# Kernel tuning notes

Measured on AMD Instinct MI355X. Metric: run time of the kernel, lower is better.

The kernel has to match this reference:

```python
import jax, jax.numpy as jnp
import numpy as np


def setup_inputs() -> dict:
    key = jax.random.key(0)
    k1, k2 = jax.random.split(key)
    decoder_output = jax.random.normal(k1, (8, 2048, 128), dtype=jnp.float32)
    encoder_output = jax.random.normal(k2, (8, 4096, 128), dtype=jnp.float32)
    return {"decoder_output": decoder_output, "encoder_output": encoder_output}


def reference(decoder_output, encoder_output):
    # Unscaled Luong (general dot) attention.
    # scores: [B, Tq, Tk] = dec [B,Tq,D] . enc [B,Tk,D]^T
    scores = jnp.einsum('bqd,bkd->bqk', decoder_output, encoder_output)
    attention = jax.nn.softmax(scores, axis=-1)
    # context: [B, Tq, D] = attn [B,Tq,Tk] . enc [B,Tk,D]
    context = jnp.einsum('bqk,bkd->bqd', attention, encoder_output)
    return (context, attention)
```

## Files before the change

### kernel.cpp

```cpp
#include <hip/hip_runtime.h>

using f16   = _Float16;
using f16x4 = __attribute__((ext_vector_type(4))) _Float16;
using f16x8 = __attribute__((ext_vector_type(8))) _Float16;
using f32x4 = __attribute__((ext_vector_type(4))) float;

#define NBATCH 8
#define TQ 2048
#define TK 4096
#define DD 128
#define QBLK 32
#define KBLK 128
#define NT (TK / KBLK)
#define CTX_ELEMS ((size_t)NBATCH * TQ * DD)
#define PWLD 56
#define CTLD 132
#define KTB 36864

__device__ __forceinline__ int koff(int t, int d) {
    const int blk = ((t >> 2) & 3) ^ ((d >> 4) & 3);
    return (t >> 4) * 2304 + (d >> 4) * 288 + blk * 72 + (t & 3) * 16 + (d & 15);
}

__device__ __forceinline__ f16x4 ds_read_tr16(unsigned addr) {
    f16x4 d;
    asm volatile("ds_read_b64_tr_b16 %0, %1" : "=v"(d) : "v"(addr));
    return d;
}

__device__ __forceinline__ void pipe_barrier() {
    asm volatile("s_waitcnt lgkmcnt(0)" ::: "memory");
    __builtin_amdgcn_s_barrier();
    __builtin_amdgcn_sched_barrier(0);
}

__global__ __launch_bounds__(256)
void cvt_kernel(const float* __restrict__ in, f16* __restrict__ out) {
    const size_t i = ((size_t)blockIdx.x * 256 + threadIdx.x) * 8;
    const float4 a = *(const float4*)(in + i);
    const float4 b = *(const float4*)(in + i + 4);
    f16x8 h;
    h[0] = (f16)a.x; h[1] = (f16)a.y; h[2] = (f16)a.z; h[3] = (f16)a.w;
    h[4] = (f16)b.x; h[5] = (f16)b.y; h[6] = (f16)b.z; h[7] = (f16)b.w;
    *(f16x8*)(out + i) = h;
}

template<bool F16SRC>
__global__ __launch_bounds__(512, 4)
void luong_attn_kernel(const float* __restrict__ dec,
                       const void* __restrict__ encv,
                       float* __restrict__ out) {
    __shared__ __align__(16) char LDSbuf[2 * KTB + 512];
    f16*   Kt0   = (f16*)LDSbuf;
    f16*   Kt1   = (f16*)(LDSbuf + KTB);
    f16*   PwAll = (f16*)(LDSbuf + KTB);
    float* Zbuf  = (float*)(LDSbuf + 2 * KTB);

    const int tid  = threadIdx.x;
    const int wid  = tid >> 6;
    const int lane = tid & 63;
    const int lo   = lane & 15;
    const int g    = lane >> 4;
    const int qg   = wid & 1;
    const int th   = wid >> 1;

    const int b     = blockIdx.x & 7;
    const int qbase = (blockIdx.x >> 3) * QBLK;

    const float* encB32 = F16SRC ? nullptr : ((const float*)encv) + (size_t)b * TK * DD;
    const f16*   encB16 = F16SRC ? ((const f16*)encv) + (size_t)b * TK * DD : nullptr;
    float* attn = out + CTX_ELEMS + ((size_t)b * TQ + qbase) * TK;

    f16x8  s16[4];
    float4 s32[8];
    auto loadR = [&](int tile) {
        if constexpr (F16SRC) {
            const f16* src = encB16 + (size_t)tile * KBLK * DD;
            #pragma unroll
            for (int i = 0; i < 4; ++i) {
                const int c = tid + (i << 9);
                s16[i] = *(const f16x8*)(src + (c >> 4) * DD + ((c & 15) << 3));
            }
        } else {
            const float* src = encB32 + (size_t)tile * KBLK * DD;
            #pragma unroll
            for (int i = 0; i < 8; ++i) {
                const int c = tid + (i << 9);
                s32[i] = *(const float4*)(src + (c >> 5) * DD + ((c & 31) << 2));
            }
        }
    };
    auto writeR = [&](f16* Kt) {
        if constexpr (F16SRC) {
            #pragma unroll
            for (int i = 0; i < 4; ++i) {
                const int c = tid + (i << 9);
                *(f16x8*)&Kt[koff(c >> 4, (c & 15) << 3)] = s16[i];
            }
        } else {
            #pragma unroll
            for (int i = 0; i < 8; ++i) {
                const int c = tid + (i << 9);
                f16x4 h;
                h[0] = (f16)s32[i].x; h[1] = (f16)s32[i].y;
                h[2] = (f16)s32[i].z; h[3] = (f16)s32[i].w;
                *(f16x4*)&Kt[koff(c >> 5, (c & 31) << 2)] = h;
            }
        }
    };

    const float* qp = dec + ((size_t)b * TQ + qbase + qg * 16 + lo) * DD;
    f16x8 qf[4];
    #pragma unroll
    for (int kk = 0; kk < 4; ++kk) {
        const float4 x = *(const float4*)(qp + kk * 32 + g * 8);
        const float4 y = *(const float4*)(qp + kk * 32 + g * 8 + 4);
        f16x8 h;
        h[0] = (f16)x.x; h[1] = (f16)x.y; h[2] = (f16)x.z; h[3] = (f16)x.w;
        h[4] = (f16)y.x; h[5] = (f16)y.y; h[6] = (f16)y.z; h[7] = (f16)y.w;
        qf[kk] = h;
    }

    float Zp[4] = {0.f, 0.f, 0.f, 0.f};
    loadR(0);
    writeR(Kt0);
    pipe_barrier();
    #pragma unroll 1
    for (int tile = 0; tile < NT; ++tile) {
        f16* Ktc = (tile & 1) ? Kt1 : Kt0;
        f16* Ktn = (tile & 1) ? Kt0 : Kt1;
        if (tile + 1 < NT) loadR(tile + 1);

        f32x4 S[2];
        #pragma unroll
        for (int f = 0; f < 2; ++f) { f32x4 z = {0.f, 0.f, 0.f, 0.f}; S[f] = z; }
        __builtin_amdgcn_s_setprio(1);
        #pragma unroll
        for (int f = 0; f < 2; ++f) {
            const int t = th * 32 + f * 16 + lo;
            #pragma unroll
            for (int kk = 0; kk < 4; ++kk) {
                const f16x8 bf = *(const f16x8*)&Ktc[koff(t, kk * 32 + g * 8)];
                S[f] = __builtin_amdgcn_mfma_f32_16x16x32_f16(qf[kk], bf, S[f], 0, 0, 0);
            }
        }
        __builtin_amdgcn_s_setprio(0);

        if (tile + 1 < NT) writeR(Ktn);
        #pragma unroll
        for (int r = 0; r < 4; ++r)
            Zp[r] += __expf(S[0][r]) + __expf(S[1][r]);
        pipe_barrier();
    }

    #pragma unroll
    for (int r = 0; r < 4; ++r) {
        Zp[r] += __shfl_xor(Zp[r], 1);
        Zp[r] += __shfl_xor(Zp[r], 2);
        Zp[r] += __shfl_xor(Zp[r], 4);
        Zp[r] += __shfl_xor(Zp[r], 8);
    }
    if (lo == 0) {
        #pragma unroll
        for (int r = 0; r < 4; ++r) Zbuf[wid * 16 + 4 * g + r] = Zp[r];
    }
    __syncthreads();
    float iz[4];
    #pragma unroll
    for (int r = 0; r < 4; ++r) {
        float z = 0.f;
        #pragma unroll
        for (int t4 = 0; t4 < 4; ++t4) z += Zbuf[(t4 * 2 + qg) * 16 + 4 * g + r];
        iz[r] = 1.0f / z;
    }
    __syncthreads();

    f32x4 ctx[8];
    #pragma unroll
    for (int n = 0; n < 8; ++n) { f32x4 z = {0.f, 0.f, 0.f, 0.f}; ctx[n] = z; }

    f16* Pw = PwAll + wid * 16 * PWLD;
    const unsigned KtBase = (unsigned)(size_t)&Kt0[0];
    const int t0 = th * 32 + g * 8;

    #pragma unroll 1
    for (int tile = 0; tile < NT; ++tile) {
        loadR(tile);
        writeR(Kt0);
        pipe_barrier();

        f32x4 S[2];
        #pragma unroll
        for (int f = 0; f < 2; ++f) { f32x4 z = {0.f, 0.f, 0.f, 0.f}; S[f] = z; }
        __builtin_amdgcn_s_setprio(1);
        #pragma unroll
        for (int f = 0; f < 2; ++f) {
            const int t = th * 32 + f * 16 + lo;
            #pragma unroll
            for (int kk = 0; kk < 4; ++kk) {
                const f16x8 bf = *(const f16x8*)&Kt0[koff(t, kk * 32 + g * 8)];
                S[f] = __builtin_amdgcn_mfma_f32_16x16x32_f16(qf[kk], bf, S[f], 0, 0, 0);
            }
        }
        __builtin_amdgcn_s_setprio(0);

        #pragma unroll
        for (int f = 0; f < 2; ++f) {
            const int tloc = f * 16 + lo;
            #pragma unroll
            for (int r = 0; r < 4; ++r)
                Pw[(4 * g + r) * PWLD + tloc] = (f16)(__expf(S[f][r]) * iz[r]);
        }
        asm volatile("" ::: "memory");

        {
            const int qq  = lane >> 2;
            const int grp = lane & 3;
            const f16x8 pr = *(const f16x8*)&Pw[qq * PWLD + grp * 8];
            f32x4 a0, a1;
            a0[0] = (float)pr[0]; a0[1] = (float)pr[1]; a0[2] = (float)pr[2]; a0[3] = (float)pr[3];
            a1[0] = (float)pr[4]; a1[1] = (float)pr[5]; a1[2] = (float)pr[6]; a1[3] = (float)pr[7];
            float* dst = attn + (size_t)(qg * 16 + qq) * TK + tile * KBLK + th * 32 + grp * 8;
            __builtin_nontemporal_store(a0, (f32x4*)dst);
            __builtin_nontemporal_store(a1, (f32x4*)(dst + 4));
        }

        const f16x8 pa = *(const f16x8*)&Pw[lo * PWLD + g * 8];
        __builtin_amdgcn_s_setprio(1);
        #pragma unroll
        for (int nh = 0; nh < 2; ++nh) {
            f16x4 tr0[4], tr1[4];
            #pragma unroll
            for (int n4 = 0; n4 < 4; ++n4) {
                const int n = nh * 4 + n4;
                const int blk0 = ((t0 >> 2) & 3) ^ (n & 3);
                const int blk1 = (((t0 + 4) >> 2) & 3) ^ (n & 3);
                const unsigned a0 =
                    KtBase + (unsigned)(((t0 >> 4) * 2304 + n * 288 + blk0 * 72) * 2) + lo * 8;
                const unsigned a1 =
                    KtBase + (unsigned)(((t0 >> 4) * 2304 + n * 288 + blk1 * 72) * 2) + lo * 8;
                tr0[n4] = ds_read_tr16(a0);
                tr1[n4] = ds_read_tr16(a1);
            }
            asm volatile("s_waitcnt lgkmcnt(0)" ::: "memory");
            __builtin_amdgcn_sched_barrier(0);
            #pragma unroll
            for (int n4 = 0; n4 < 4; ++n4) {
                f16x8 vb;
                vb[0] = tr0[n4][0]; vb[1] = tr0[n4][1]; vb[2] = tr0[n4][2]; vb[3] = tr0[n4][3];
                vb[4] = tr1[n4][0]; vb[5] = tr1[n4][1]; vb[6] = tr1[n4][2]; vb[7] = tr1[n4][3];
                ctx[nh * 4 + n4] =
                    __builtin_amdgcn_mfma_f32_16x16x32_f16(pa, vb, ctx[nh * 4 + n4], 0, 0, 0);
            }
        }
        __builtin_amdgcn_s_setprio(0);
        pipe_barrier();
    }

    float* CT = (float*)LDSbuf;
    const int q32 = qg * 16 + 4 * g;
    if (th >= 2) {
        #pragma unroll
        for (int n = 0; n < 8; ++n)
            #pragma unroll
            for (int r = 0; r < 4; ++r)
                CT[((th - 2) * 32 + q32 + r) * CTLD + n * 16 + lo] = ctx[n][r];
    }
    __syncthreads();
    if (th < 2) {
        #pragma unroll
        for (int n = 0; n < 8; ++n)
            #pragma unroll
            for (int r = 0; r < 4; ++r)
                ctx[n][r] += CT[(th * 32 + q32 + r) * CTLD + n * 16 + lo];
    }
    __syncthreads();
    if (th == 1) {
        #pragma unroll
        for (int n = 0; n < 8; ++n)
            #pragma unroll
            for (int r = 0; r < 4; ++r)
                CT[(q32 + r) * CTLD + n * 16 + lo] = ctx[n][r];
    }
    __syncthreads();
    if (th == 0) {
        #pragma unroll
        for (int n = 0; n < 8; ++n)
            #pragma unroll
            for (int r = 0; r < 4; ++r)
                out[((size_t)b * TQ + qbase + q32 + r) * DD + n * 16 + lo] =
                    ctx[n][r] + CT[(q32 + r) * CTLD + n * 16 + lo];
    }
}

extern "C" void kernel_launch(void* const* d_in, const int* in_sizes, int n_in,
                              void* d_out, int out_size, void* d_ws, size_t ws_size,
                              hipStream_t stream) {
    (void)in_sizes; (void)n_in; (void)out_size;
    const float* dec = (const float*)d_in[0];
    const float* enc = (const float*)d_in[1];
    float* out = (float*)d_out;
    dim3 grid(NBATCH * (TQ / QBLK));
    dim3 block(512);

    const size_t encN = (size_t)NBATCH * TK * DD;
    if (ws_size >= encN * sizeof(f16)) {
        f16* encH = (f16*)d_ws;
        hipLaunchKernelGGL(cvt_kernel, dim3((unsigned)(encN / (256 * 8))), dim3(256),
                           0, stream, enc, encH);
        hipLaunchKernelGGL((luong_attn_kernel<true>), grid, block, 0, stream,
                           dec, (const void*)encH, out);
    } else {
        hipLaunchKernelGGL((luong_attn_kernel<false>), grid, block, 0, stream,
                           dec, (const void*)enc, out);
    }
}
```

Measured before the change: 122.7 us.

## Reuse K fragments across both query halves and prefetch next tile in pass two

In the normalizer pass, each wave now covers 16 keys for both 16-row query halves. Each K fragment read from LDS therefore feeds two MFMAs instead of being read once per query half. In the second pass, the global load of the next K tile is issued after the score computation rather than at the top of the loop, and the first tile's load is started before the Z reduction; one barrier after the reduction is dropped. This should cut LDS traffic in pass one and hide global-load latency in pass two, at the cost of extra registers for the duplicated query fragments and a larger Z buffer.

New measurement: 152.0 us. 1.24x slower.

```diff
diff --git a/kernel.cpp b/kernel.cpp
--- a/kernel.cpp
+++ b/kernel.cpp
@@ -50,7 +50,7 @@
 void luong_attn_kernel(const float* __restrict__ dec,
                        const void* __restrict__ encv,
                        float* __restrict__ out) {
-    __shared__ __align__(16) char LDSbuf[2 * KTB + 512];
+    __shared__ __align__(16) char LDSbuf[2 * KTB + 1024];
     f16*   Kt0   = (f16*)LDSbuf;
     f16*   Kt1   = (f16*)(LDSbuf + KTB);
     f16*   PwAll = (f16*)(LDSbuf + KTB);
@@ -109,19 +109,27 @@
         }
     };
 
-    const float* qp = dec + ((size_t)b * TQ + qbase + qg * 16 + lo) * DD;
-    f16x8 qf[4];
-    #pragma unroll
-    for (int kk = 0; kk < 4; ++kk) {
-        const float4 x = *(const float4*)(qp + kk * 32 + g * 8);
-        const float4 y = *(const float4*)(qp + kk * 32 + g * 8 + 4);
-        f16x8 h;
-        h[0] = (f16)x.x; h[1] = (f16)x.y; h[2] = (f16)x.z; h[3] = (f16)x.w;
-        h[4] = (f16)y.x; h[5] = (f16)y.y; h[6] = (f16)y.z; h[7] = (f16)y.w;
-        qf[kk] = h;
-    }
-
-    float Zp[4] = {0.f, 0.f, 0.f, 0.f};
+    f16x8 qfh[2][4];
+    #pragma unroll
+    for (int h2 = 0; h2 < 2; ++h2) {
+        const float* qp = dec + ((size_t)b * TQ + qbase + h2 * 16 + lo) * DD;
+        #pragma unroll
+        for (int kk = 0; kk < 4; ++kk) {
+            const float4 x = *(const float4*)(qp + kk * 32 + g * 8);
+            const float4 y = *(const float4*)(qp + kk * 32 + g * 8 + 4);
+            f16x8 h;
+            h[0] = (f16)x.x; h[1] = (f16)x.y; h[2] = (f16)x.z; h[3] = (f16)x.w;
+            h[4] = (f16)y.x; h[5] = (f16)y.y; h[6] = (f16)y.z; h[7] = (f16)y.w;
+            qfh[h2][kk] = h;
+        }
+    }
+
+    float Zp[2][4];
+    #pragma unroll
+    for (int h2 = 0; h2 < 2; ++h2)
+        #pragma unroll
+        for (int r = 0; r < 4; ++r) Zp[h2][r] = 0.f;
+
     loadR(0);
     writeR(Kt0);
     pipe_barrier();
@@ -131,38 +139,44 @@
         f16* Ktn = (tile & 1) ? Kt0 : Kt1;
         if (tile + 1 < NT) loadR(tile + 1);
 
-        f32x4 S[2];
-        #pragma unroll
-        for (int f = 0; f < 2; ++f) { f32x4 z = {0.f, 0.f, 0.f, 0.f}; S[f] = z; }
+        f32x4 S0 = {0.f, 0.f, 0.f, 0.f};
+        f32x4 S1 = {0.f, 0.f, 0.f, 0.f};
+        const int t = wid * 16 + lo;
         __builtin_amdgcn_s_setprio(1);
         #pragma unroll
-        for (int f = 0; f < 2; ++f) {
-            const int t = th * 32 + f * 16 + lo;
-            #pragma unroll
-            for (int kk = 0; kk < 4; ++kk) {
-                const f16x8 bf = *(const f16x8*)&Ktc[koff(t, kk * 32 + g * 8)];
-                S[f] = __builtin_amdgcn_mfma_f32_16x16x32_f16(qf[kk], bf, S[f], 0, 0, 0);
-            }
+        for (int kk = 0; kk < 4; ++kk) {
+            const f16x8 bf = *(const f16x8*)&Ktc[koff(t, kk * 32 + g * 8)];
+            S0 = __builtin_amdgcn_mfma_f32_16x16x32_f16(qfh[0][kk], bf, S0, 0, 0, 0);
+            S1 = __builtin_amdgcn_mfma_f32_16x16x32_f16(qfh[1][kk], bf, S1, 0, 0, 0);
         }
         __builtin_amdgcn_s_setprio(0);
 
         if (tile + 1 < NT) writeR(Ktn);
         #pragma unroll
-        for (int r = 0; r < 4; ++r)
-            Zp[r] += __expf(S[0][r]) + __expf(S[1][r]);
+        for (int r = 0; r < 4; ++r) {
+            Zp[0][r] += __expf(S0[r]);
+            Zp[1][r] += __expf(S1[r]);
+        }
         pipe_barrier();
     }
 
-    #pragma unroll
-    for (int r = 0; r < 4; ++r) {
-        Zp[r] += __shfl_xor(Zp[r], 1);
-        Zp[r] += __shfl_xor(Zp[r], 2);
-        Zp[r] += __shfl_xor(Zp[r], 4);
-        Zp[r] += __shfl_xor(Zp[r], 8);
-    }
+    loadR(0);
+
+    #pragma unroll
+    for (int h2 = 0; h2 < 2; ++h2)
+        #pragma unroll
+        for (int r = 0; r < 4; ++r) {
+            Zp[h2][r] += __shfl_xor(Zp[h2][r], 1);
+            Zp[h2][r] += __shfl_xor(Zp[h2][r], 2);
+            Zp[h2][r] += __shfl_xor(Zp[h2][r], 4);
+            Zp[h2][r] += __shfl_xor(Zp[h2][r], 8);
+        }
     if (lo == 0) {
         #pragma unroll
-        for (int r = 0; r < 4; ++r) Zbuf[wid * 16 + 4 * g + r] = Zp[r];
+        for (int h2 = 0; h2 < 2; ++h2)
+            #pragma unroll
+            for (int r = 0; r < 4; ++r)
+                Zbuf[wid * 32 + h2 * 16 + 4 * g + r] = Zp[h2][r];
     }
     __syncthreads();
     float iz[4];
@@ -170,10 +184,9 @@
     for (int r = 0; r < 4; ++r) {
         float z = 0.f;
         #pragma unroll
-        for (int t4 = 0; t4 < 4; ++t4) z += Zbuf[(t4 * 2 + qg) * 16 + 4 * g + r];
+        for (int w = 0; w < 8; ++w) z += Zbuf[w * 32 + qg * 16 + 4 * g + r];
         iz[r] = 1.0f / z;
     }
-    __syncthreads();
 
     f32x4 ctx[8];
     #pragma unroll
@@ -185,7 +198,6 @@
 
     #pragma unroll 1
     for (int tile = 0; tile < NT; ++tile) {
-        loadR(tile);
         writeR(Kt0);
         pipe_barrier();
 
@@ -199,7 +211,7 @@
             #pragma unroll
             for (int kk = 0; kk < 4; ++kk) {
                 const f16x8 bf = *(const f16x8*)&Kt0[koff(t, kk * 32 + g * 8)];
-                S[f] = __builtin_amdgcn_mfma_f32_16x16x32_f16(qf[kk], bf, S[f], 0, 0, 0);
+                S[f] = __builtin_amdgcn_mfma_f32_16x16x32_f16(qfh[qg][kk], bf, S[f], 0, 0, 0);
             }
         }
         __builtin_amdgcn_s_setprio(0);
@@ -225,6 +237,8 @@
             __builtin_nontemporal_store(a1, (f32x4*)(dst + 4));
         }
 
+        if (tile + 1 < NT) loadR(tile + 1);
+
         const f16x8 pa = *(const f16x8*)&Pw[lo * PWLD + g * 8];
         __builtin_amdgcn_s_setprio(1);
         #pragma unroll
```
